# Optimization experiments

Measured on AMD Instinct MI355X. Metric: run time of the kernel, lower is better.

The kernel has to match this reference:

```python
import jax, jax.numpy as jnp
import numpy as np

EMBED_DIM = 1024
NUM_HEADS = 16
HEAD_DIM = EMBED_DIM // NUM_HEADS


def setup_inputs() -> dict:
    key = jax.random.key(0)
    ks = jax.random.split(key, 9)
    B, S, D = 4, 2048, EMBED_DIM
    scale = 1.0 / np.sqrt(D)
    inp = {
        "x": jax.random.normal(ks[0], (B, S, D), dtype=jnp.float32),
        "wq": jax.random.normal(ks[1], (D, D), dtype=jnp.float32) * scale,
        "bq": jnp.zeros((D,), dtype=jnp.float32),
        "wk": jax.random.normal(ks[2], (D, D), dtype=jnp.float32) * scale,
        "bk": jnp.zeros((D,), dtype=jnp.float32),
        "wv": jax.random.normal(ks[3], (D, D), dtype=jnp.float32) * scale,
        "bv": jnp.zeros((D,), dtype=jnp.float32),
        "wo": jax.random.normal(ks[4], (D, D), dtype=jnp.float32) * scale,
        "bo": jnp.zeros((D,), dtype=jnp.float32),
    }
    return inp


def reference(x, wq, bq, wk, bk, wv, bv, wo, bo):
    B, S, D = x.shape
    H, Hd = NUM_HEADS, HEAD_DIM

    def split_heads(t):
        # [B, S, D] -> [B, H, S, Hd]
        return t.reshape(B, S, H, Hd).transpose(0, 2, 1, 3)

    q = split_heads(x @ wq.T + bq)
    k = split_heads(x @ wk.T + bk)
    v = split_heads(x @ wv.T + bv)

    scores = jnp.einsum("bhqd,bhkd->bhqk", q, k) / jnp.sqrt(jnp.float32(Hd))
    attn = jax.nn.softmax(scores, axis=-1)
    out = jnp.einsum("bhqk,bhkd->bhqd", attn, v)  # [B, H, S, Hd]
    out = out.transpose(0, 2, 1, 3).reshape(B, S, D)
    return out @ wo.T + bo
```

## Files before the change

kernel.cpp:

```cpp
#include <hip/hip_runtime.h>
#include <hip/hip_bf16.h>
#include <hip/hip_fp16.h>

typedef _Float16 f16;
typedef f16 f16x8 __attribute__((ext_vector_type(8)));
typedef f16 f16x4 __attribute__((ext_vector_type(4)));
typedef f16 f16x2 __attribute__((ext_vector_type(2)));
typedef float f32x4 __attribute__((ext_vector_type(4)));
typedef float f32x16 __attribute__((ext_vector_type(16)));
typedef unsigned int u32x4 __attribute__((ext_vector_type(4)));
typedef unsigned int u32x2 __attribute__((ext_vector_type(2)));

#define MFMA16(a, b, c) __builtin_amdgcn_mfma_f32_16x16x32_f16(a, b, c, 0, 0, 0)
#define MFMA32(a, b, c) __builtin_amdgcn_mfma_f32_32x32x16_f16(a, b, c, 0, 0, 0)

constexpr int BB = 4, SS = 2048, DD = 1024, HH = 16, HDIM = 64;
constexpr int MM = BB * SS;
constexpr float QSCALE = 0.125f * 1.44269504088896340736f;


__device__ __forceinline__ void gl_lds16(const void* g, void* l) {
  __builtin_amdgcn_global_load_lds((const __attribute__((address_space(1))) void*)g,
                                   (__attribute__((address_space(3))) void*)l, 16, 0, 0);
}

__global__ __launch_bounds__(256) void cvt_all_kernel(const float* __restrict__ x,
                                                      const float* __restrict__ w0,
                                                      const float* __restrict__ w1,
                                                      const float* __restrict__ w2,
                                                      const float* __restrict__ w3,
                                                      f16* xh, f16* o0, f16* o1,
                                                      f16* o2, f16* o3) {
  int bid = blockIdx.x;
  const float* in; f16* out; int idx;
  if (bid < MM * DD / 4 / 256) {
    in = x; out = xh; idx = bid * 256 + threadIdx.x;
  } else {
    int wb = bid - MM * DD / 4 / 256;
    int which = wb >> 10;
    in = which == 0 ? w0 : which == 1 ? w1 : which == 2 ? w2 : w3;
    out = which == 0 ? o0 : which == 1 ? o1 : which == 2 ? o2 : o3;
    idx = (wb & 1023) * 256 + threadIdx.x;
  }
  f32x4 v = reinterpret_cast<const f32x4*>(in)[idx];
  f16x4 o;
  o[0] = (f16)v[0]; o[1] = (f16)v[1]; o[2] = (f16)v[2]; o[3] = (f16)v[3];
  reinterpret_cast<f16x4*>(out)[idx] = o;
}

template <bool QKV>
__global__ __launch_bounds__(512) void gemm8_kernel(const f16* __restrict__ A,
                                                    const f16* __restrict__ W0,
                                                    const f16* __restrict__ W1,
                                                    const f16* __restrict__ W2,
                                                    const float* __restrict__ b0,
                                                    const float* __restrict__ b1,
                                                    const float* __restrict__ b2,
                                                    void* __restrict__ O0,
                                                    void* __restrict__ O1,
                                                    void* __restrict__ O2) {
  constexpr int NT = 16;
  constexpr int BUF = 256 * 64 + 128 * 64;
  __shared__ __align__(16) f16 smem[3 * BUF];

  const int p = blockIdx.x;
  const int bl = p >> 3;
  const int NS = QKV ? 24 : 8;
  const int nn = bl % NS;
  const int my = (p & 7) + 8 * (bl / NS);
  const int mat = QKV ? (nn >> 3) : 0;
  const int m0 = my * 256;
  const int n0 = (nn & 7) * 128;

  const f16* W = mat == 0 ? W0 : (mat == 1 ? W1 : W2);
  const float* bias = mat == 0 ? b0 : (mat == 1 ? b1 : b2);

  const int tid = threadIdx.x;
  const int w = tid >> 6, lane = tid & 63;
  const int wm = w >> 2, wn = w & 3;
  const int g = lane >> 4, r = lane & 15;

  const int srow_a = ((w * 64 + lane) >> 3);
  const int sc = lane & 7;

  f32x4 acc[8][2] = {};

#define STAGE_A(I, PB, KT)                                                              \
  do {                                                                                  \
    int cid_ = ((I)*8 + w) * 64 + lane;                                                 \
    int row_ = cid_ >> 3, c_ = cid_ & 7;                                                \
    gl_lds16(A + (size_t)(m0 + row_) * 1024 + (KT) + ((c_ ^ (row_ & 7)) << 3),          \
             smem + (PB) + ((I)*8 + w) * 512);                                          \
  } while (0)
#define STAGE_B(I, PB, KT)                                                              \
  do {                                                                                  \
    int cid_ = ((I)*8 + w) * 64 + lane;                                                 \
    int row_ = cid_ >> 3, c_ = cid_ & 7;                                                \
    gl_lds16(W + (size_t)(n0 + row_) * 1024 + (KT) + ((c_ ^ (row_ & 7)) << 3),          \
             smem + (PB) + 256 * 64 + ((I)*8 + w) * 512);                               \
  } while (0)

#pragma unroll
  for (int i = 0; i < 4; ++i) STAGE_A(i, 0, 0);
#pragma unroll
  for (int i = 0; i < 2; ++i) STAGE_B(i, 0, 0);
#pragma unroll
  for (int i = 0; i < 4; ++i) STAGE_A(i, BUF, 64);
#pragma unroll
  for (int i = 0; i < 2; ++i) STAGE_B(i, BUF, 64);
  __builtin_amdgcn_sched_barrier(0);
  asm volatile("s_waitcnt vmcnt(6)" ::: "memory");
  __builtin_amdgcn_s_barrier();
  __builtin_amdgcn_sched_barrier(0);

  for (int t = 0; t < NT; ++t) {
    const f16* Ab = smem + (t % 3) * BUF;
    const f16* Wb = Ab + 256 * 64;
    const int pb = ((t + 2) % 3) * BUF;
    const int kpf = (t + 2) * 64;
    const bool do_pf = (t + 2) < NT;

    f16x8 wf[2][2];
#pragma unroll
    for (int ks = 0; ks < 2; ++ks)
#pragma unroll
      for (int j = 0; j < 2; ++j) {
        int rowW = wn * 32 + j * 16 + r;
        wf[ks][j] = *reinterpret_cast<const f16x8*>(
            Wb + rowW * 64 + (((ks << 2) | g) ^ (rowW & 7)) * 8);
      }

    if (do_pf) { STAGE_A(0, pb, kpf); STAGE_A(1, pb, kpf); STAGE_B(0, pb, kpf); }
    __builtin_amdgcn_s_setprio(1);
#pragma unroll
    for (int ks = 0; ks < 2; ++ks)
#pragma unroll
      for (int i = 0; i < 4; ++i) {
        int rowA = wm * 128 + i * 16 + r;
        f16x8 af = *reinterpret_cast<const f16x8*>(
            Ab + rowA * 64 + (((ks << 2) | g) ^ (rowA & 7)) * 8);
        acc[i][0] = MFMA16(af, wf[ks][0], acc[i][0]);
        acc[i][1] = MFMA16(af, wf[ks][1], acc[i][1]);
      }
    __builtin_amdgcn_s_setprio(0);

    if (do_pf) { STAGE_A(2, pb, kpf); STAGE_A(3, pb, kpf); STAGE_B(1, pb, kpf); }
    __builtin_amdgcn_s_setprio(1);
#pragma unroll
    for (int ks = 0; ks < 2; ++ks)
#pragma unroll
      for (int i = 0; i < 4; ++i) {
        int rowA = wm * 128 + 64 + i * 16 + r;
        f16x8 af = *reinterpret_cast<const f16x8*>(
            Ab + rowA * 64 + (((ks << 2) | g) ^ (rowA & 7)) * 8);
        acc[4 + i][0] = MFMA16(af, wf[ks][0], acc[4 + i][0]);
        acc[4 + i][1] = MFMA16(af, wf[ks][1], acc[4 + i][1]);
      }
    __builtin_amdgcn_s_setprio(0);

    __builtin_amdgcn_sched_barrier(0);
    if (t < NT - 2) {
      asm volatile("s_waitcnt vmcnt(6)" ::: "memory");
      __builtin_amdgcn_s_barrier();
    } else if (t == NT - 2) {
      asm volatile("s_waitcnt vmcnt(0)" ::: "memory");
      __builtin_amdgcn_s_barrier();
    }
    __builtin_amdgcn_sched_barrier(0);
  }
#undef STAGE_A
#undef STAGE_B

  const int sbase = m0 & 2047, bb = m0 >> 11;
  if constexpr (!QKV) {
    float* Out = reinterpret_cast<float*>(O0);
#pragma unroll
    for (int ii = 0; ii < 8; ++ii) {
      int rowoff = (ii >> 2) * 64 + (ii & 3) * 16;
#pragma unroll
      for (int j = 0; j < 2; ++j)
#pragma unroll
        for (int q = 0; q < 4; ++q) {
          int gm = m0 + wm * 128 + rowoff + g * 4 + q;
          int gn = n0 + wn * 32 + j * 16 + r;
          Out[(size_t)gm * 1024 + gn] = acc[ii][j][q] + bias[gn];
        }
    }
  } else if (mat == 0) {
    f16* Qo = reinterpret_cast<f16*>(O0);
#pragma unroll
    for (int ii = 0; ii < 8; ++ii) {
      int rowoff = (ii >> 2) * 64 + (ii & 3) * 16;
#pragma unroll
      for (int j = 0; j < 2; ++j)
#pragma unroll
        for (int q = 0; q < 4; ++q) {
          int gm = m0 + wm * 128 + rowoff + g * 4 + q;
          int gn = n0 + wn * 32 + j * 16 + r;
          float v = (acc[ii][j][q] + bias[gn]) * QSCALE;
          int b = gm >> 11, s = gm & 2047;
          int hh = gn >> 6, hd = gn & 63;
          Qo[(((size_t)(b * HH + hh)) * SS + s) * HDIM + hd] = (f16)v;
        }
    }
  } else if (mat == 1) {
    f16* Ko = reinterpret_cast<f16*>(O1);
    __syncthreads();
    f16* T = smem;
#pragma unroll
    for (int ii = 0; ii < 8; ++ii) {
      int rowoff = (ii >> 2) * 64 + (ii & 3) * 16;
#pragma unroll
      for (int j = 0; j < 2; ++j)
#pragma unroll
        for (int q = 0; q < 4; ++q) {
          int ml = wm * 128 + rowoff + g * 4 + q;
          int nl = wn * 32 + j * 16 + r;
          T[ml * 136 + nl] = (f16)(acc[ii][j][q] + bias[n0 + nl]);
        }
    }
    __syncthreads();
#pragma unroll
    for (int it = 0; it < 8; ++it) {
      int cid = it * 512 + tid;
      int row_s = cid & 255, ns = cid >> 8;
      u32x4 v = *reinterpret_cast<const u32x4*>(T + row_s * 136 + ns * 8);
      int gn0 = n0 + ns * 8;
      int hh = gn0 >> 6, slot = (gn0 & 63) >> 3;
      int tile = (sbase >> 6) + (row_s >> 6), row = row_s & 63;
      size_t off = ((((size_t)(bb * HH + hh) * 32 + tile) * 8 + slot) * 64 + row) * 8;
      *reinterpret_cast<u32x4*>(Ko + off) = v;
    }
  } else {
    f16* Vo = reinterpret_cast<f16*>(O2);
    __syncthreads();
    f16* T = smem;
#pragma unroll
    for (int ii = 0; ii < 8; ++ii) {
      int rowoff = (ii >> 2) * 64 + (ii & 3) * 16;
#pragma unroll
      for (int j = 0; j < 2; ++j)
#pragma unroll
        for (int q = 0; q < 4; ++q) {
          int ml = wm * 128 + rowoff + g * 4 + q;
          int nl = wn * 32 + j * 16 + r;
          T[nl * 264 + ml] = (f16)(acc[ii][j][q] + bias[n0 + nl]);
        }
    }
    __syncthreads();
#pragma unroll
    for (int it = 0; it < 8; ++it) {
      int cid = it * 512 + tid;
      int hd_l = cid & 127, rest = cid >> 7;
      int sl = rest & 7, tl = rest >> 3;
      u32x4 v = *reinterpret_cast<const u32x4*>(T + hd_l * 264 + tl * 64 + sl * 8);
      int gn = n0 + hd_l, hh = gn >> 6, hd = gn & 63;
      int tile = (sbase >> 6) + tl;
      size_t off = ((((size_t)(bb * HH + hh) * 32 + tile) * 8 + sl) * 64 + hd) * 8;
      *reinterpret_cast<u32x4*>(Vo + off) = v;
    }
  }
}

__global__ __launch_bounds__(256, 2) void attn_kernel(const f16* __restrict__ Q,
                                                      const f16* __restrict__ K,
                                                      const f16* __restrict__ Vt,
                                                      f16* __restrict__ AO) {
  __shared__ __align__(16) f16 Kls[2][8 * 512];
  __shared__ __align__(16) f16 Vls[3][8 * 512];
  __shared__ __align__(16) float Lw[4][64];

  const int p = blockIdx.x;
  const int qx = (p >> 3) & 7;
  const int bh = (p & 7) | ((p >> 6) << 3);
  const int q0 = qx * 256;

  const int tid = threadIdx.x;
  const int w = tid >> 6, lane = tid & 63;
  const int q31 = lane & 31;
  const int h = lane >> 5;
  const f16* Kg = K + (size_t)bh * (SS * HDIM);
  const f16* Vg = Vt + (size_t)bh * (SS * HDIM);
  const int s0 = 2 * w;
  const int rofs = h * 512 + q31 * 8;

  const f16* Qg = Q + ((size_t)bh * SS + q0 + w * 64 + q31) * HDIM + 8 * h;
  f16x8 qf[2][4];
#pragma unroll
  for (int f = 0; f < 2; ++f)
#pragma unroll
    for (int m = 0; m < 4; ++m)
      qf[f][m] = *reinterpret_cast<const f16x8*>(Qg + f * 32 * HDIM + 16 * m);

  f32x16 oacc[2][2] = {};
  float lsum0 = 0.f, lsum1 = 0.f;
  unsigned pkP0[8], pkP1[8];

#pragma unroll
  for (int i = 0; i < 2; ++i) {
    int s_idx = s0 + i;
    gl_lds16(Kg + (size_t)(s_idx * 64 + lane) * 8, &Kls[0][s_idx * 512]);
    gl_lds16(Vg + (size_t)(s_idx * 64 + lane) * 8, &Vls[0][s_idx * 512]);
  }
  __syncthreads();

#define QK_PHASE(KC, KB, SC0, SC1)                                                   \
  do {                                                                               \
    _Pragma("unroll") for (int m = 0; m < 4; ++m) {                                  \
      f16x8 kf = *reinterpret_cast<const f16x8*>((KC) + m * 1024 + (KB)*256 + rofs); \
      SC0 = MFMA32(kf, qf[0][m], SC0);                                               \
      SC1 = MFMA32(kf, qf[1][m], SC1);                                               \
    }                                                                                \
  } while (0)

#define PV_PHASE(VPTR, JB)                                                               \
  do {                                                                                   \
    _Pragma("unroll") for (int jl = 0; jl < 2; ++jl) {                                   \
      auto a0 = __builtin_amdgcn_permlane32_swap(pkP0[4 * jl + 0], pkP0[4 * jl + 2],     \
                                                 false, false);                          \
      auto a1 = __builtin_amdgcn_permlane32_swap(pkP0[4 * jl + 1], pkP0[4 * jl + 3],     \
                                                 false, false);                          \
      u32x4 fa = {(unsigned)a0[0], (unsigned)a1[0], (unsigned)a0[1], (unsigned)a1[1]};   \
      f16x8 pa0 = __builtin_bit_cast(f16x8, fa);                                         \
      auto b0 = __builtin_amdgcn_permlane32_swap(pkP1[4 * jl + 0], pkP1[4 * jl + 2],     \
                                                 false, false);                          \
      auto b1 = __builtin_amdgcn_permlane32_swap(pkP1[4 * jl + 1], pkP1[4 * jl + 3],     \
                                                 false, false);                          \
      u32x4 fb = {(unsigned)b0[0], (unsigned)b1[0], (unsigned)b0[1], (unsigned)b1[1]};   \
      f16x8 pa1 = __builtin_bit_cast(f16x8, fb);                                         \
      const int j = (JB) + jl;                                                           \
      _Pragma("unroll") for (int vb = 0; vb < 2; ++vb) {                                 \
        f16x8 vbf = *reinterpret_cast<const f16x8*>((VPTR) + j * 1024 + vb * 256 + rofs);\
        oacc[0][vb] = MFMA32(pa0, vbf, oacc[0][vb]);                                     \
        oacc[1][vb] = MFMA32(pa1, vbf, oacc[1][vb]);                                     \
      }                                                                                  \
    }                                                                                    \
  } while (0)

#define SM_PHASE(SC0, SC1)                                                               \
  do {                                                                                   \
    _Pragma("unroll") for (int rp = 0; rp < 4; ++rp)                                     \
        _Pragma("unroll") for (int pp = 0; pp < 2; ++pp) {                               \
      float a0 = __builtin_amdgcn_exp2f((SC0)[4 * rp + 2 * pp]);                         \
      float a1 = __builtin_amdgcn_exp2f((SC0)[4 * rp + 2 * pp + 1]);                     \
      pkP0[2 * rp + pp] = __builtin_bit_cast(unsigned, __builtin_amdgcn_cvt_pkrtz(a0, a1));\
      float b0 = __builtin_amdgcn_exp2f((SC1)[4 * rp + 2 * pp]);                         \
      float b1 = __builtin_amdgcn_exp2f((SC1)[4 * rp + 2 * pp + 1]);                     \
      pkP1[2 * rp + pp] = __builtin_bit_cast(unsigned, __builtin_amdgcn_cvt_pkrtz(b0, b1));\
    }                                                                                    \
    {                                                                                    \
      f16x2 u01 = __builtin_bit_cast(f16x2, pkP0[0]) + __builtin_bit_cast(f16x2, pkP0[1]);\
      f16x2 u23 = __builtin_bit_cast(f16x2, pkP0[2]) + __builtin_bit_cast(f16x2, pkP0[3]);\
      f16x2 u45 = __builtin_bit_cast(f16x2, pkP0[4]) + __builtin_bit_cast(f16x2, pkP0[5]);\
      f16x2 u67 = __builtin_bit_cast(f16x2, pkP0[6]) + __builtin_bit_cast(f16x2, pkP0[7]);\
      f16x2 ut = (u01 + u23) + (u45 + u67);                                              \
      lsum0 += (float)ut[0] + (float)ut[1];                                              \
    }                                                                                    \
    {                                                                                    \
      f16x2 u01 = __builtin_bit_cast(f16x2, pkP1[0]) + __builtin_bit_cast(f16x2, pkP1[1]);\
      f16x2 u23 = __builtin_bit_cast(f16x2, pkP1[2]) + __builtin_bit_cast(f16x2, pkP1[3]);\
      f16x2 u45 = __builtin_bit_cast(f16x2, pkP1[4]) + __builtin_bit_cast(f16x2, pkP1[5]);\
      f16x2 u67 = __builtin_bit_cast(f16x2, pkP1[6]) + __builtin_bit_cast(f16x2, pkP1[7]);\
      f16x2 ut = (u01 + u23) + (u45 + u67);                                              \
      lsum1 += (float)ut[0] + (float)ut[1];                                              \
    }                                                                                    \
  } while (0)

  for (int t = 0; t < SS / 64; ++t) {
    if (t < SS / 64 - 1) {
      f16* kdst = &Kls[(t + 1) & 1][0];
      f16* vdst = &Vls[(t + 1) % 3][0];
#pragma unroll
      for (int i = 0; i < 2; ++i) {
        int s_idx = s0 + i;
        gl_lds16(Kg + (size_t)((t + 1) * 512 + s_idx * 64 + lane) * 8, kdst + s_idx * 512);
        gl_lds16(Vg + (size_t)((t + 1) * 512 + s_idx * 64 + lane) * 8, vdst + s_idx * 512);
      }
    }
    const f16* Kc = &Kls[t & 1][0];
    const f16* Vcur = &Vls[t % 3][0];
    const f16* Vprev = &Vls[(t + 2) % 3][0];

    {
      f32x16 sc0 = {}, sc1 = {};
      __builtin_amdgcn_s_setprio(1);
      QK_PHASE(Kc, 0, sc0, sc1);
      if (t > 0) PV_PHASE(Vprev, 2);
      __builtin_amdgcn_s_setprio(0);
      SM_PHASE(sc0, sc1);
    }
    {
      f32x16 sc0 = {}, sc1 = {};
      __builtin_amdgcn_s_setprio(1);
      QK_PHASE(Kc, 1, sc0, sc1);
      PV_PHASE(Vcur, 0);
      __builtin_amdgcn_s_setprio(0);
      SM_PHASE(sc0, sc1);
    }
    __syncthreads();
  }

  {
    const f16* Vlast = &Vls[(SS / 64 - 1) % 3][0];
    __builtin_amdgcn_s_setprio(1);
    PV_PHASE(Vlast, 2);
    __builtin_amdgcn_s_setprio(0);
  }

  lsum0 += __shfl_xor(lsum0, 32, 64);
  lsum1 += __shfl_xor(lsum1, 32, 64);
  if (h == 0) {
    Lw[w][q31] = 1.0f / lsum0;
    Lw[w][32 + q31] = 1.0f / lsum1;
  }

  const int b = bh >> 4, head = bh & 15;
#pragma unroll
  for (int f = 0; f < 2; ++f) {
    f32x4 li[4];
#pragma unroll
    for (int rq = 0; rq < 4; ++rq)
      li[rq] = *reinterpret_cast<const f32x4*>(&Lw[w][32 * f + 8 * rq + 4 * h]);
    f16* aobase = AO + ((size_t)(b * SS + q0 + 64 * w + 32 * f)) * DD + head * 64 + q31;
#pragma unroll
    for (int vb = 0; vb < 2; ++vb)
#pragma unroll
      for (int reg = 0; reg < 16; ++reg) {
        int q = (reg & 3) + 8 * (reg >> 2) + 4 * h;
        aobase[(size_t)q * DD + 32 * vb] = (f16)(oacc[f][vb][reg] * li[reg >> 2][reg & 3]);
      }
  }
#undef QK_PHASE
#undef PV_PHASE
#undef SM_PHASE
}

extern "C" void kernel_launch(void* const* d_in, const int* in_sizes, int n_in,
                              void* d_out, int out_size, void* d_ws, size_t ws_size,
                              hipStream_t stream) {
  (void)in_sizes; (void)n_in; (void)out_size; (void)ws_size;
  const float* x  = (const float*)d_in[0];
  const float* wq = (const float*)d_in[1];
  const float* bq = (const float*)d_in[2];
  const float* wk = (const float*)d_in[3];
  const float* bk = (const float*)d_in[4];
  const float* wv = (const float*)d_in[5];
  const float* bv = (const float*)d_in[6];
  const float* wo = (const float*)d_in[7];
  const float* bo = (const float*)d_in[8];
  float* out = (float*)d_out;

  char* ws = (char*)d_ws;
  f16* xh  = (f16*)ws; ws += (size_t)MM * DD * 2;
  f16* wqh = (f16*)ws; ws += (size_t)DD * DD * 2;
  f16* wkh = (f16*)ws; ws += (size_t)DD * DD * 2;
  f16* wvh = (f16*)ws; ws += (size_t)DD * DD * 2;
  f16* woh = (f16*)ws; ws += (size_t)DD * DD * 2;
  f16* Qb  = (f16*)ws; ws += (size_t)MM * DD * 2;
  f16* Kb  = (f16*)ws; ws += (size_t)MM * DD * 2;
  f16* Vtb = (f16*)ws; ws += (size_t)MM * DD * 2;
  f16* AOb = (f16*)ws; ws += (size_t)MM * DD * 2;

  cvt_all_kernel<<<MM * DD / 4 / 256 + 4 * (DD * DD / 4 / 256), 256, 0, stream>>>(
      x, wq, wk, wv, wo, xh, wqh, wkh, wvh, woh);

  gemm8_kernel<true><<<768, 512, 0, stream>>>(xh, wqh, wkh, wvh, bq, bk, bv, Qb, Kb, Vtb);

  attn_kernel<<<512, 256, 0, stream>>>(Qb, Kb, Vtb, AOb);

  gemm8_kernel<false><<<256, 512, 0, stream>>>(AOb, woh, nullptr, nullptr, bo, nullptr,
                                               nullptr, out, nullptr, nullptr);
}
```

Baseline: 180.0 us.

## Split attention waves into two software-pipeline schedules to stagger softmax and MFMA

```diff
diff --git a/kernel.cpp b/kernel.cpp
--- a/kernel.cpp
+++ b/kernel.cpp
@@ -17,7 +17,6 @@
 constexpr int BB = 4, SS = 2048, DD = 1024, HH = 16, HDIM = 64;
 constexpr int MM = BB * SS;
 constexpr float QSCALE = 0.125f * 1.44269504088896340736f;
-
 
 __device__ __forceinline__ void gl_lds16(const void* g, void* l) {
   __builtin_amdgcn_global_load_lds((const __attribute__((address_space(1))) void*)g,
@@ -80,9 +79,6 @@
   const int wm = w >> 2, wn = w & 3;
   const int g = lane >> 4, r = lane & 15;
 
-  const int srow_a = ((w * 64 + lane) >> 3);
-  const int sc = lane & 7;
-
   f32x4 acc[8][2] = {};
 
 #define STAGE_A(I, PB, KT)                                                              \
@@ -294,7 +290,6 @@
 
   f32x16 oacc[2][2] = {};
   float lsum0 = 0.f, lsum1 = 0.f;
-  unsigned pkP0[8], pkP1[8];
 
 #pragma unroll
   for (int i = 0; i < 2; ++i) {
@@ -303,6 +298,17 @@
     gl_lds16(Vg + (size_t)(s_idx * 64 + lane) * 8, &Vls[0][s_idx * 512]);
   }
   __syncthreads();
+
+#define STAGE_T(T1)                                                                      \
+  do {                                                                                   \
+    f16* kdst = &Kls[(T1)&1][0];                                                         \
+    f16* vdst = &Vls[(T1) % 3][0];                                                       \
+    _Pragma("unroll") for (int i = 0; i < 2; ++i) {                                      \
+      int s_idx = s0 + i;                                                                \
+      gl_lds16(Kg + (size_t)((T1)*512 + s_idx * 64 + lane) * 8, kdst + s_idx * 512);     \
+      gl_lds16(Vg + (size_t)((T1)*512 + s_idx * 64 + lane) * 8, vdst + s_idx * 512);     \
+    }                                                                                    \
+  } while (0)
 
 #define QK_PHASE(KC, KB, SC0, SC1)                                                   \
   do {                                                                               \
@@ -313,18 +319,18 @@
     }                                                                                \
   } while (0)
 
-#define PV_PHASE(VPTR, JB)                                                               \
+#define PV_PHASE(PK0, PK1, VPTR, JB)                                                     \
   do {                                                                                   \
     _Pragma("unroll") for (int jl = 0; jl < 2; ++jl) {                                   \
-      auto a0 = __builtin_amdgcn_permlane32_swap(pkP0[4 * jl + 0], pkP0[4 * jl + 2],     \
+      auto a0 = __builtin_amdgcn_permlane32_swap((PK0)[4 * jl + 0], (PK0)[4 * jl + 2],   \
                                                  false, false);                          \
-      auto a1 = __builtin_amdgcn_permlane32_swap(pkP0[4 * jl + 1], pkP0[4 * jl + 3],     \
+      auto a1 = __builtin_amdgcn_permlane32_swap((PK0)[4 * jl + 1], (PK0)[4 * jl + 3],   \
                                                  false, false);                          \
       u32x4 fa = {(unsigned)a0[0], (unsigned)a1[0], (unsigned)a0[1], (unsigned)a1[1]};   \
       f16x8 pa0 = __builtin_bit_cast(f16x8, fa);                                         \
-      auto b0 = __builtin_amdgcn_permlane32_swap(pkP1[4 * jl + 0], pkP1[4 * jl + 2],     \
+      auto b0 = __builtin_amdgcn_permlane32_swap((PK1)[4 * jl + 0], (PK1)[4 * jl + 2],   \
                                                  false, false);                          \
-      auto b1 = __builtin_amdgcn_permlane32_swap(pkP1[4 * jl + 1], pkP1[4 * jl + 3],     \
+      auto b1 = __builtin_amdgcn_permlane32_swap((PK1)[4 * jl + 1], (PK1)[4 * jl + 3],   \
                                                  false, false);                          \
       u32x4 fb = {(unsigned)b0[0], (unsigned)b1[0], (unsigned)b0[1], (unsigned)b1[1]};   \
       f16x8 pa1 = __builtin_bit_cast(f16x8, fb);                                         \
@@ -337,74 +343,101 @@
     }                                                                                    \
   } while (0)
 
-#define SM_PHASE(SC0, SC1)                                                               \
+#define SM_PHASE(SC0, SC1, PK0, PK1)                                                     \
   do {                                                                                   \
     _Pragma("unroll") for (int rp = 0; rp < 4; ++rp)                                     \
         _Pragma("unroll") for (int pp = 0; pp < 2; ++pp) {                               \
       float a0 = __builtin_amdgcn_exp2f((SC0)[4 * rp + 2 * pp]);                         \
       float a1 = __builtin_amdgcn_exp2f((SC0)[4 * rp + 2 * pp + 1]);                     \
-      pkP0[2 * rp + pp] = __builtin_bit_cast(unsigned, __builtin_amdgcn_cvt_pkrtz(a0, a1));\
+      (PK0)[2 * rp + pp] = __builtin_bit_cast(unsigned, __builtin_amdgcn_cvt_pkrtz(a0, a1));\
       float b0 = __builtin_amdgcn_exp2f((SC1)[4 * rp + 2 * pp]);                         \
       float b1 = __builtin_amdgcn_exp2f((SC1)[4 * rp + 2 * pp + 1]);                     \
-      pkP1[2 * rp + pp] = __builtin_bit_cast(unsigned, __builtin_amdgcn_cvt_pkrtz(b0, b1));\
+      (PK1)[2 * rp + pp] = __builtin_bit_cast(unsigned, __builtin_amdgcn_cvt_pkrtz(b0, b1));\
     }                                                                                    \
     {                                                                                    \
-      f16x2 u01 = __builtin_bit_cast(f16x2, pkP0[0]) + __builtin_bit_cast(f16x2, pkP0[1]);\
-      f16x2 u23 = __builtin_bit_cast(f16x2, pkP0[2]) + __builtin_bit_cast(f16x2, pkP0[3]);\
-      f16x2 u45 = __builtin_bit_cast(f16x2, pkP0[4]) + __builtin_bit_cast(f16x2, pkP0[5]);\
-      f16x2 u67 = __builtin_bit_cast(f16x2, pkP0[6]) + __builtin_bit_cast(f16x2, pkP0[7]);\
+      f16x2 u01 = __builtin_bit_cast(f16x2, (PK0)[0]) + __builtin_bit_cast(f16x2, (PK0)[1]);\
+      f16x2 u23 = __builtin_bit_cast(f16x2, (PK0)[2]) + __builtin_bit_cast(f16x2, (PK0)[3]);\
+      f16x2 u45 = __builtin_bit_cast(f16x2, (PK0)[4]) + __builtin_bit_cast(f16x2, (PK0)[5]);\
+      f16x2 u67 = __builtin_bit_cast(f16x2, (PK0)[6]) + __builtin_bit_cast(f16x2, (PK0)[7]);\
       f16x2 ut = (u01 + u23) + (u45 + u67);                                              \
       lsum0 += (float)ut[0] + (float)ut[1];                                              \
     }                                                                                    \
     {                                                                                    \
-      f16x2 u01 = __builtin_bit_cast(f16x2, pkP1[0]) + __builtin_bit_cast(f16x2, pkP1[1]);\
-      f16x2 u23 = __builtin_bit_cast(f16x2, pkP1[2]) + __builtin_bit_cast(f16x2, pkP1[3]);\
-      f16x2 u45 = __builtin_bit_cast(f16x2, pkP1[4]) + __builtin_bit_cast(f16x2, pkP1[5]);\
-      f16x2 u67 = __builtin_bit_cast(f16x2, pkP1[6]) + __builtin_bit_cast(f16x2, pkP1[7]);\
+      f16x2 u01 = __builtin_bit_cast(f16x2, (PK1)[0]) + __builtin_bit_cast(f16x2, (PK1)[1]);\
+      f16x2 u23 = __builtin_bit_cast(f16x2, (PK1)[2]) + __builtin_bit_cast(f16x2, (PK1)[3]);\
+      f16x2 u45 = __builtin_bit_cast(f16x2, (PK1)[4]) + __builtin_bit_cast(f16x2, (PK1)[5]);\
+      f16x2 u67 = __builtin_bit_cast(f16x2, (PK1)[6]) + __builtin_bit_cast(f16x2, (PK1)[7]);\
       f16x2 ut = (u01 + u23) + (u45 + u67);                                              \
       lsum1 += (float)ut[0] + (float)ut[1];                                              \
     }                                                                                    \
   } while (0)
 
-  for (int t = 0; t < SS / 64; ++t) {
-    if (t < SS / 64 - 1) {
-      f16* kdst = &Kls[(t + 1) & 1][0];
-      f16* vdst = &Vls[(t + 1) % 3][0];
-#pragma unroll
-      for (int i = 0; i < 2; ++i) {
-        int s_idx = s0 + i;
-        gl_lds16(Kg + (size_t)((t + 1) * 512 + s_idx * 64 + lane) * 8, kdst + s_idx * 512);
-        gl_lds16(Vg + (size_t)((t + 1) * 512 + s_idx * 64 + lane) * 8, vdst + s_idx * 512);
-      }
-    }
-    const f16* Kc = &Kls[t & 1][0];
-    const f16* Vcur = &Vls[t % 3][0];
-    const f16* Vprev = &Vls[(t + 2) % 3][0];
-
+  if (w < 2) {
+    unsigned pkP0[8], pkP1[8];
+    for (int t = 0; t < SS / 64; ++t) {
+      if (t < SS / 64 - 1) STAGE_T(t + 1);
+      const f16* Kc = &Kls[t & 1][0];
+      const f16* Vcur = &Vls[t % 3][0];
+      const f16* Vprev = &Vls[(t + 2) % 3][0];
+      {
+        f32x16 sc0 = {}, sc1 = {};
+        __builtin_amdgcn_s_setprio(1);
+        QK_PHASE(Kc, 0, sc0, sc1);
+        if (t > 0) PV_PHASE(pkP0, pkP1, Vprev, 2);
+        __builtin_amdgcn_s_setprio(0);
+        SM_PHASE(sc0, sc1, pkP0, pkP1);
+      }
+      {
+        f32x16 sc0 = {}, sc1 = {};
+        __builtin_amdgcn_s_setprio(1);
+        QK_PHASE(Kc, 1, sc0, sc1);
+        PV_PHASE(pkP0, pkP1, Vcur, 0);
+        __builtin_amdgcn_s_setprio(0);
+        SM_PHASE(sc0, sc1, pkP0, pkP1);
+      }
+      __syncthreads();
+    }
     {
-      f32x16 sc0 = {}, sc1 = {};
+      const f16* Vlast = &Vls[(SS / 64 - 1) % 3][0];
       __builtin_amdgcn_s_setprio(1);
-      QK_PHASE(Kc, 0, sc0, sc1);
-      if (t > 0) PV_PHASE(Vprev, 2);
+      PV_PHASE(pkP0, pkP1, Vlast, 2);
       __builtin_amdgcn_s_setprio(0);
-      SM_PHASE(sc0, sc1);
-    }
+    }
+  } else {
+    f32x16 sA0, sA1, sB0, sB1;
+    unsigned pkA0[8], pkA1[8], pkB0[8], pkB1[8];
+    for (int t = 0; t < SS / 64; ++t) {
+      if (t < SS / 64 - 1) STAGE_T(t + 1);
+      const f16* Kc = &Kls[t & 1][0];
+      const f16* Vm1 = &Vls[(t + 2) % 3][0];
+      if (t > 0) SM_PHASE(sB0, sB1, pkB0, pkB1);
+      {
+        f32x16 n0v = {}, n1v = {};
+        sA0 = n0v; sA1 = n1v;
+        __builtin_amdgcn_s_setprio(1);
+        QK_PHASE(Kc, 0, sA0, sA1);
+        if (t > 0) PV_PHASE(pkA0, pkA1, Vm1, 0);
+        __builtin_amdgcn_s_setprio(0);
+      }
+      SM_PHASE(sA0, sA1, pkA0, pkA1);
+      {
+        f32x16 n0v = {}, n1v = {};
+        sB0 = n0v; sB1 = n1v;
+        __builtin_amdgcn_s_setprio(1);
+        QK_PHASE(Kc, 1, sB0, sB1);
+        if (t > 0) PV_PHASE(pkB0, pkB1, Vm1, 2);
+        __builtin_amdgcn_s_setprio(0);
+      }
+      __syncthreads();
+    }
+    SM_PHASE(sB0, sB1, pkB0, pkB1);
     {
-      f32x16 sc0 = {}, sc1 = {};
+      const f16* Vlast = &Vls[(SS / 64 - 1) % 3][0];
       __builtin_amdgcn_s_setprio(1);
-      QK_PHASE(Kc, 1, sc0, sc1);
-      PV_PHASE(Vcur, 0);
+      PV_PHASE(pkA0, pkA1, Vlast, 0);
+      PV_PHASE(pkB0, pkB1, Vlast, 2);
       __builtin_amdgcn_s_setprio(0);
-      SM_PHASE(sc0, sc1);
-    }
-    __syncthreads();
-  }
-
-  {
-    const f16* Vlast = &Vls[(SS / 64 - 1) % 3][0];
-    __builtin_amdgcn_s_setprio(1);
-    PV_PHASE(Vlast, 2);
-    __builtin_amdgcn_s_setprio(0);
+    }
   }
 
   lsum0 += __shfl_xor(lsum0, 32, 64);
@@ -430,6 +463,7 @@
         aobase[(size_t)q * DD + 32 * vb] = (f16)(oacc[f][vb][reg] * li[reg >> 2][reg & 3]);
       }
   }
+#undef STAGE_T
 #undef QK_PHASE
 #undef PV_PHASE
 #undef SM_PHASE
```

Result: no change. 181.0 us (+0.6%).

## Split attention KV range across waves and merge partial outputs in LDS

Applied to the files above, without the earlier changes.

```diff
diff --git a/kernel.cpp b/kernel.cpp
--- a/kernel.cpp
+++ b/kernel.cpp
@@ -17,7 +17,6 @@
 constexpr int BB = 4, SS = 2048, DD = 1024, HH = 16, HDIM = 64;
 constexpr int MM = BB * SS;
 constexpr float QSCALE = 0.125f * 1.44269504088896340736f;
-
 
 __device__ __forceinline__ void gl_lds16(const void* g, void* l) {
   __builtin_amdgcn_global_load_lds((const __attribute__((address_space(1))) void*)g,
@@ -80,9 +79,6 @@
   const int wm = w >> 2, wn = w & 3;
   const int g = lane >> 4, r = lane & 15;
 
-  const int srow_a = ((w * 64 + lane) >> 3);
-  const int sc = lane & 7;
-
   f32x4 acc[8][2] = {};
 
 #define STAGE_A(I, PB, KT)                                                              \
@@ -262,29 +258,46 @@
   }
 }
 
-__global__ __launch_bounds__(256, 2) void attn_kernel(const f16* __restrict__ Q,
+__global__ __launch_bounds__(256, 4) void attn_kernel(const f16* __restrict__ Q,
                                                       const f16* __restrict__ K,
                                                       const f16* __restrict__ Vt,
                                                       f16* __restrict__ AO) {
-  __shared__ __align__(16) f16 Kls[2][8 * 512];
-  __shared__ __align__(16) f16 Vls[3][8 * 512];
-  __shared__ __align__(16) float Lw[4][64];
+  __shared__ __align__(16) char stg_raw[32768];
+  __shared__ float Lpart[2][64];
+  __shared__ float Lw[2][64];
 
   const int p = blockIdx.x;
-  const int qx = (p >> 3) & 7;
-  const int bh = (p & 7) | ((p >> 6) << 3);
-  const int q0 = qx * 256;
+  const int qx = (p >> 3) & 15;
+  const int bh = (p & 7) | ((p >> 7) << 3);
+  const int q0 = qx * 128;
 
   const int tid = threadIdx.x;
   const int w = tid >> 6, lane = tid & 63;
-  const int q31 = lane & 31;
-  const int h = lane >> 5;
-  const f16* Kg = K + (size_t)bh * (SS * HDIM);
-  const f16* Vg = Vt + (size_t)bh * (SS * HDIM);
-  const int s0 = 2 * w;
-  const int rofs = h * 512 + q31 * 8;
-
-  const f16* Qg = Q + ((size_t)bh * SS + q0 + w * 64 + q31) * HDIM + 8 * h;
+  const int qg = w & 1, kh = w >> 1;
+  const int q31 = lane & 31, h = lane >> 5;
+
+  f16* stgp = (f16*)stg_raw;
+#define STG(KH, KV, B) (stgp + (((KH)*2 + (KV)) * 2 + (B)) * 2048)
+
+  const f16* KVg = (qg == 0 ? K : Vt) + (size_t)bh * (SS * HDIM);
+
+#define STAGE_U(U, B)                                                                   \
+  do {                                                                                  \
+    int T_ = kh * 16 + ((U) >> 1), h2_ = (U)&1;                                         \
+    if (qg == 0) {                                                                      \
+      _Pragma("unroll") for (int i = 0; i < 4; ++i) {                                   \
+        gl_lds16(KVg + ((size_t)(T_ * 8 + 2 * i + h) * 64 + 32 * h2_ + q31) * 8,        \
+                 STG(kh, 0, B) + i * 512);                                              \
+      }                                                                                 \
+    } else {                                                                            \
+      _Pragma("unroll") for (int i = 0; i < 4; ++i) {                                   \
+        gl_lds16(KVg + ((size_t)(T_ * 8 + 4 * h2_ + i) * 64 + lane) * 8,                \
+                 STG(kh, 1, B) + i * 512);                                              \
+      }                                                                                 \
+    }                                                                                   \
+  } while (0)
+
+  const f16* Qg = Q + ((size_t)bh * SS + q0 + qg * 64 + q31) * HDIM + 8 * h;
   f16x8 qf[2][4];
 #pragma unroll
   for (int f = 0; f < 2; ++f)
@@ -294,145 +307,128 @@
 
   f32x16 oacc[2][2] = {};
   float lsum0 = 0.f, lsum1 = 0.f;
-  unsigned pkP0[8], pkP1[8];
-
-#pragma unroll
-  for (int i = 0; i < 2; ++i) {
-    int s_idx = s0 + i;
-    gl_lds16(Kg + (size_t)(s_idx * 64 + lane) * 8, &Kls[0][s_idx * 512]);
-    gl_lds16(Vg + (size_t)(s_idx * 64 + lane) * 8, &Vls[0][s_idx * 512]);
-  }
+  const int rofsK = h * 256 + q31 * 8;
+  const int rofsV = h * 512 + q31 * 8;
+
+  STAGE_U(0, 0);
   __syncthreads();
 
-#define QK_PHASE(KC, KB, SC0, SC1)                                                   \
-  do {                                                                               \
-    _Pragma("unroll") for (int m = 0; m < 4; ++m) {                                  \
-      f16x8 kf = *reinterpret_cast<const f16x8*>((KC) + m * 1024 + (KB)*256 + rofs); \
-      SC0 = MFMA32(kf, qf[0][m], SC0);                                               \
-      SC1 = MFMA32(kf, qf[1][m], SC1);                                               \
-    }                                                                                \
-  } while (0)
-
-#define PV_PHASE(VPTR, JB)                                                               \
-  do {                                                                                   \
-    _Pragma("unroll") for (int jl = 0; jl < 2; ++jl) {                                   \
-      auto a0 = __builtin_amdgcn_permlane32_swap(pkP0[4 * jl + 0], pkP0[4 * jl + 2],     \
-                                                 false, false);                          \
-      auto a1 = __builtin_amdgcn_permlane32_swap(pkP0[4 * jl + 1], pkP0[4 * jl + 3],     \
-                                                 false, false);                          \
-      u32x4 fa = {(unsigned)a0[0], (unsigned)a1[0], (unsigned)a0[1], (unsigned)a1[1]};   \
-      f16x8 pa0 = __builtin_bit_cast(f16x8, fa);                                         \
-      auto b0 = __builtin_amdgcn_permlane32_swap(pkP1[4 * jl + 0], pkP1[4 * jl + 2],     \
-                                                 false, false);                          \
-      auto b1 = __builtin_amdgcn_permlane32_swap(pkP1[4 * jl + 1], pkP1[4 * jl + 3],     \
-                                                 false, false);                          \
-      u32x4 fb = {(unsigned)b0[0], (unsigned)b1[0], (unsigned)b0[1], (unsigned)b1[1]};   \
-      f16x8 pa1 = __builtin_bit_cast(f16x8, fb);                                         \
-      const int j = (JB) + jl;                                                           \
-      _Pragma("unroll") for (int vb = 0; vb < 2; ++vb) {                                 \
-        f16x8 vbf = *reinterpret_cast<const f16x8*>((VPTR) + j * 1024 + vb * 256 + rofs);\
-        oacc[0][vb] = MFMA32(pa0, vbf, oacc[0][vb]);                                     \
-        oacc[1][vb] = MFMA32(pa1, vbf, oacc[1][vb]);                                     \
-      }                                                                                  \
-    }                                                                                    \
-  } while (0)
-
-#define SM_PHASE(SC0, SC1)                                                               \
-  do {                                                                                   \
-    _Pragma("unroll") for (int rp = 0; rp < 4; ++rp)                                     \
-        _Pragma("unroll") for (int pp = 0; pp < 2; ++pp) {                               \
-      float a0 = __builtin_amdgcn_exp2f((SC0)[4 * rp + 2 * pp]);                         \
-      float a1 = __builtin_amdgcn_exp2f((SC0)[4 * rp + 2 * pp + 1]);                     \
-      pkP0[2 * rp + pp] = __builtin_bit_cast(unsigned, __builtin_amdgcn_cvt_pkrtz(a0, a1));\
-      float b0 = __builtin_amdgcn_exp2f((SC1)[4 * rp + 2 * pp]);                         \
-      float b1 = __builtin_amdgcn_exp2f((SC1)[4 * rp + 2 * pp + 1]);                     \
-      pkP1[2 * rp + pp] = __builtin_bit_cast(unsigned, __builtin_amdgcn_cvt_pkrtz(b0, b1));\
-    }                                                                                    \
-    {                                                                                    \
-      f16x2 u01 = __builtin_bit_cast(f16x2, pkP0[0]) + __builtin_bit_cast(f16x2, pkP0[1]);\
-      f16x2 u23 = __builtin_bit_cast(f16x2, pkP0[2]) + __builtin_bit_cast(f16x2, pkP0[3]);\
-      f16x2 u45 = __builtin_bit_cast(f16x2, pkP0[4]) + __builtin_bit_cast(f16x2, pkP0[5]);\
-      f16x2 u67 = __builtin_bit_cast(f16x2, pkP0[6]) + __builtin_bit_cast(f16x2, pkP0[7]);\
-      f16x2 ut = (u01 + u23) + (u45 + u67);                                              \
-      lsum0 += (float)ut[0] + (float)ut[1];                                              \
-    }                                                                                    \
-    {                                                                                    \
-      f16x2 u01 = __builtin_bit_cast(f16x2, pkP1[0]) + __builtin_bit_cast(f16x2, pkP1[1]);\
-      f16x2 u23 = __builtin_bit_cast(f16x2, pkP1[2]) + __builtin_bit_cast(f16x2, pkP1[3]);\
-      f16x2 u45 = __builtin_bit_cast(f16x2, pkP1[4]) + __builtin_bit_cast(f16x2, pkP1[5]);\
-      f16x2 u67 = __builtin_bit_cast(f16x2, pkP1[6]) + __builtin_bit_cast(f16x2, pkP1[7]);\
-      f16x2 ut = (u01 + u23) + (u45 + u67);                                              \
-      lsum1 += (float)ut[0] + (float)ut[1];                                              \
-    }                                                                                    \
-  } while (0)
-
-  for (int t = 0; t < SS / 64; ++t) {
-    if (t < SS / 64 - 1) {
-      f16* kdst = &Kls[(t + 1) & 1][0];
-      f16* vdst = &Vls[(t + 1) % 3][0];
-#pragma unroll
-      for (int i = 0; i < 2; ++i) {
-        int s_idx = s0 + i;
-        gl_lds16(Kg + (size_t)((t + 1) * 512 + s_idx * 64 + lane) * 8, kdst + s_idx * 512);
-        gl_lds16(Vg + (size_t)((t + 1) * 512 + s_idx * 64 + lane) * 8, vdst + s_idx * 512);
+  for (int u = 0; u < 32; ++u) {
+    if (u < 31) STAGE_U(u + 1, (u + 1) & 1);
+    const f16* Kb = STG(kh, 0, u & 1);
+    const f16* Vb = STG(kh, 1, u & 1);
+
+    f32x16 sc0 = {}, sc1 = {};
+    __builtin_amdgcn_s_setprio(1);
+#pragma unroll
+    for (int m = 0; m < 4; ++m) {
+      f16x8 kf = *reinterpret_cast<const f16x8*>(Kb + m * 512 + rofsK);
+      sc0 = MFMA32(kf, qf[0][m], sc0);
+      sc1 = MFMA32(kf, qf[1][m], sc1);
+    }
+    __builtin_amdgcn_s_setprio(0);
+
+    unsigned pk0[8], pk1[8];
+#pragma unroll
+    for (int rp = 0; rp < 4; ++rp)
+#pragma unroll
+      for (int pp = 0; pp < 2; ++pp) {
+        float a0 = __builtin_amdgcn_exp2f(sc0[4 * rp + 2 * pp]);
+        float a1 = __builtin_amdgcn_exp2f(sc0[4 * rp + 2 * pp + 1]);
+        pk0[2 * rp + pp] = __builtin_bit_cast(unsigned, __builtin_amdgcn_cvt_pkrtz(a0, a1));
+        float b0 = __builtin_amdgcn_exp2f(sc1[4 * rp + 2 * pp]);
+        float b1 = __builtin_amdgcn_exp2f(sc1[4 * rp + 2 * pp + 1]);
+        pk1[2 * rp + pp] = __builtin_bit_cast(unsigned, __builtin_amdgcn_cvt_pkrtz(b0, b1));
       }
-    }
-    const f16* Kc = &Kls[t & 1][0];
-    const f16* Vcur = &Vls[t % 3][0];
-    const f16* Vprev = &Vls[(t + 2) % 3][0];
-
     {
-      f32x16 sc0 = {}, sc1 = {};
-      __builtin_amdgcn_s_setprio(1);
-      QK_PHASE(Kc, 0, sc0, sc1);
-      if (t > 0) PV_PHASE(Vprev, 2);
-      __builtin_amdgcn_s_setprio(0);
-      SM_PHASE(sc0, sc1);
+      f16x2 u01 = __builtin_bit_cast(f16x2, pk0[0]) + __builtin_bit_cast(f16x2, pk0[1]);
+      f16x2 u23 = __builtin_bit_cast(f16x2, pk0[2]) + __builtin_bit_cast(f16x2, pk0[3]);
+      f16x2 u45 = __builtin_bit_cast(f16x2, pk0[4]) + __builtin_bit_cast(f16x2, pk0[5]);
+      f16x2 u67 = __builtin_bit_cast(f16x2, pk0[6]) + __builtin_bit_cast(f16x2, pk0[7]);
+      f16x2 ut = (u01 + u23) + (u45 + u67);
+      lsum0 += (float)ut[0] + (float)ut[1];
     }
     {
-      f32x16 sc0 = {}, sc1 = {};
-      __builtin_amdgcn_s_setprio(1);
-      QK_PHASE(Kc, 1, sc0, sc1);
-      PV_PHASE(Vcur, 0);
-      __builtin_amdgcn_s_setprio(0);
-      SM_PHASE(sc0, sc1);
-    }
+      f16x2 u01 = __builtin_bit_cast(f16x2, pk1[0]) + __builtin_bit_cast(f16x2, pk1[1]);
+      f16x2 u23 = __builtin_bit_cast(f16x2, pk1[2]) + __builtin_bit_cast(f16x2, pk1[3]);
+      f16x2 u45 = __builtin_bit_cast(f16x2, pk1[4]) + __builtin_bit_cast(f16x2, pk1[5]);
+      f16x2 u67 = __builtin_bit_cast(f16x2, pk1[6]) + __builtin_bit_cast(f16x2, pk1[7]);
+      f16x2 ut = (u01 + u23) + (u45 + u67);
+      lsum1 += (float)ut[0] + (float)ut[1];
+    }
+
+    __builtin_amdgcn_s_setprio(1);
+#pragma unroll
+    for (int j = 0; j < 2; ++j) {
+      auto a0 = __builtin_amdgcn_permlane32_swap(pk0[4 * j + 0], pk0[4 * j + 2], false, false);
+      auto a1 = __builtin_amdgcn_permlane32_swap(pk0[4 * j + 1], pk0[4 * j + 3], false, false);
+      u32x4 fa = {(unsigned)a0[0], (unsigned)a1[0], (unsigned)a0[1], (unsigned)a1[1]};
+      f16x8 pa0 = __builtin_bit_cast(f16x8, fa);
+      auto b0 = __builtin_amdgcn_permlane32_swap(pk1[4 * j + 0], pk1[4 * j + 2], false, false);
+      auto b1 = __builtin_amdgcn_permlane32_swap(pk1[4 * j + 1], pk1[4 * j + 3], false, false);
+      u32x4 fb = {(unsigned)b0[0], (unsigned)b1[0], (unsigned)b0[1], (unsigned)b1[1]};
+      f16x8 pa1 = __builtin_bit_cast(f16x8, fb);
+#pragma unroll
+      for (int vb = 0; vb < 2; ++vb) {
+        f16x8 vbf = *reinterpret_cast<const f16x8*>(Vb + j * 1024 + vb * 256 + rofsV);
+        oacc[0][vb] = MFMA32(pa0, vbf, oacc[0][vb]);
+        oacc[1][vb] = MFMA32(pa1, vbf, oacc[1][vb]);
+      }
+    }
+    __builtin_amdgcn_s_setprio(0);
+
     __syncthreads();
-  }
-
-  {
-    const f16* Vlast = &Vls[(SS / 64 - 1) % 3][0];
-    __builtin_amdgcn_s_setprio(1);
-    PV_PHASE(Vlast, 2);
-    __builtin_amdgcn_s_setprio(0);
   }
 
   lsum0 += __shfl_xor(lsum0, 32, 64);
   lsum1 += __shfl_xor(lsum1, 32, 64);
-  if (h == 0) {
-    Lw[w][q31] = 1.0f / lsum0;
-    Lw[w][32 + q31] = 1.0f / lsum1;
-  }
-
-  const int b = bh >> 4, head = bh & 15;
-#pragma unroll
-  for (int f = 0; f < 2; ++f) {
-    f32x4 li[4];
-#pragma unroll
-    for (int rq = 0; rq < 4; ++rq)
-      li[rq] = *reinterpret_cast<const f32x4*>(&Lw[w][32 * f + 8 * rq + 4 * h]);
-    f16* aobase = AO + ((size_t)(b * SS + q0 + 64 * w + 32 * f)) * DD + head * 64 + q31;
-#pragma unroll
-    for (int vb = 0; vb < 2; ++vb)
-#pragma unroll
-      for (int reg = 0; reg < 16; ++reg) {
-        int q = (reg & 3) + 8 * (reg >> 2) + 4 * h;
-        aobase[(size_t)q * DD + 32 * vb] = (f16)(oacc[f][vb][reg] * li[reg >> 2][reg & 3]);
-      }
-  }
-#undef QK_PHASE
-#undef PV_PHASE
-#undef SM_PHASE
+
+  float* Opart = (float*)stg_raw;
+  if (kh == 1) {
+    if (h == 0) {
+      Lpart[qg][q31] = lsum0;
+      Lpart[qg][32 + q31] = lsum1;
+    }
+#pragma unroll
+    for (int f = 0; f < 2; ++f)
+#pragma unroll
+      for (int vb = 0; vb < 2; ++vb)
+#pragma unroll
+        for (int reg = 0; reg < 16; ++reg) {
+          int ql = 32 * f + (reg & 3) + 8 * (reg >> 2) + 4 * h;
+          Opart[(qg * 64 + ql) * 64 + 32 * vb + q31] = oacc[f][vb][reg];
+        }
+  }
+  __syncthreads();
+
+  if (kh == 0) {
+    lsum0 += Lpart[qg][q31];
+    lsum1 += Lpart[qg][32 + q31];
+    if (h == 0) {
+      Lw[qg][q31] = 1.0f / lsum0;
+      Lw[qg][32 + q31] = 1.0f / lsum1;
+    }
+    const int b = bh >> 4, head = bh & 15;
+#pragma unroll
+    for (int f = 0; f < 2; ++f) {
+      f32x4 li[4];
+#pragma unroll
+      for (int rq = 0; rq < 4; ++rq)
+        li[rq] = *reinterpret_cast<const f32x4*>(&Lw[qg][32 * f + 8 * rq + 4 * h]);
+      f16* aobase = AO + ((size_t)(b * SS + q0 + 64 * qg + 32 * f)) * DD + head * 64 + q31;
+#pragma unroll
+      for (int vb = 0; vb < 2; ++vb)
+#pragma unroll
+        for (int reg = 0; reg < 16; ++reg) {
+          int ql = 32 * f + (reg & 3) + 8 * (reg >> 2) + 4 * h;
+          int q = (reg & 3) + 8 * (reg >> 2) + 4 * h;
+          float v = oacc[f][vb][reg] + Opart[(qg * 64 + ql) * 64 + 32 * vb + q31];
+          aobase[(size_t)q * DD + 32 * vb] = (f16)(v * li[reg >> 2][reg & 3]);
+        }
+    }
+  }
+#undef STG
+#undef STAGE_U
 }
 
 extern "C" void kernel_launch(void* const* d_in, const int* in_sizes, int n_in,
@@ -466,7 +462,7 @@
 
   gemm8_kernel<true><<<768, 512, 0, stream>>>(xh, wqh, wkh, wvh, bq, bk, bv, Qb, Kb, Vtb);
 
-  attn_kernel<<<512, 256, 0, stream>>>(Qb, Kb, Vtb, AOb);
+  attn_kernel<<<1024, 256, 0, stream>>>(Qb, Kb, Vtb, AOb);
 
   gemm8_kernel<false><<<256, 512, 0, stream>>>(AOb, woh, nullptr, nullptr, bo, nullptr,
                                                nullptr, out, nullptr, nullptr);
```

Result: slower. 244.4 us (+35.8%).
